# Optimization experiments

Measured on AMD Instinct MI355X. Metric: run time of the kernel, lower is better.

The kernel has to match this reference:

```python
import jax, jax.numpy as jnp
import numpy as np

N_NOTE = 14  # undefined global in original; must equal output_size for one-hot feedback


def setup_inputs() -> dict:
    key = jax.random.key(0)
    ks = jax.random.split(key, 9)
    B, T, H, O = 256, 512, 2048, 14
    s_i = 1.0 / np.sqrt(14)
    s_h = 1.0 / np.sqrt(H)
    return {
        "encoder_outputs": jax.random.normal(ks[0], (B, 1, H), jnp.float32),
        "encoder_hidden": jax.random.normal(ks[1], (1, B, H), jnp.float32),
        "target_tensor": jax.random.uniform(ks[2], (B, T, O), jnp.float32),
        "W_ih": jax.random.normal(ks[3], (3 * H, 14), jnp.float32) * s_i,
        "W_hh": jax.random.normal(ks[4], (3 * H, H), jnp.float32) * s_h,
        "b_ih": jax.random.normal(ks[5], (3 * H,), jnp.float32) * s_h,
        "b_hh": jax.random.normal(ks[6], (3 * H,), jnp.float32) * s_h,
        "W_out": jax.random.normal(ks[7], (O, H), jnp.float32) * s_h,
        "b_out": jax.random.normal(ks[8], (O,), jnp.float32) * s_h,
    }


def _decode(encoder_hidden, target_tensor, W_ih, W_hh, b_ih, b_hh, W_out, b_out):
    B, T, O = target_tensor.shape
    H = W_hh.shape[1]

    def step(carry, _):
        h, x = carry  # h: [B,H], x: [B,14]
        xr = jax.nn.relu(x)
        gi = xr @ W_ih.T + b_ih            # [B,3H]
        gh = h @ W_hh.T + b_hh             # [B,3H]
        r = jax.nn.sigmoid(gi[:, :H] + gh[:, :H])
        z = jax.nn.sigmoid(gi[:, H:2 * H] + gh[:, H:2 * H])
        n = jnp.tanh(gi[:, 2 * H:] + r * gh[:, 2 * H:])
        h_new = (1.0 - z) * n + z * h
        logits = h_new @ W_out.T + b_out   # [B,O]
        # feedback: one-hot of argmax; the Python `break` in the original zeros
        # every batch element at-or-after the first hit of n_note-1
        topi = jnp.argmax(logits, axis=-1)                     # [B]
        hit = (topi == N_NOTE - 1).astype(jnp.int32)
        alive = (jnp.cumsum(hit) == 0).astype(logits.dtype)    # inclusive cumsum
        x_next = jax.nn.one_hot(topi, O, dtype=logits.dtype) * alive[:, None]
        return (h_new, x_next), logits

    h0 = encoder_hidden[0]          # [B,H]
    x0 = target_tensor[:, 0]        # [B,14] first-step input
    (h_final, _), logits = jax.lax.scan(step, (h0, x0), None, length=T)
    logits = jnp.transpose(logits, (1, 0, 2))  # [B,T,O]
    log_probs = jax.nn.log_softmax(logits, axis=-1)
    return log_probs, h_final[None]  # ([B,T,O], [1,B,H])


def reference(encoder_outputs, encoder_hidden, target_tensor, W_ih, W_hh, b_ih, b_hh, W_out, b_out):
    # encoder_outputs is accepted but unused, matching the original forward
    return _decode(encoder_hidden, target_tensor, W_ih, W_hh, b_ih, b_hh, W_out, b_out)
```

## Files before the change

kernel.cpp:

```cpp
#include <hip/hip_runtime.h>
#include <math.h>

typedef float f4 __attribute__((ext_vector_type(4)));
typedef _Float16 f16x8 __attribute__((ext_vector_type(8)));
typedef _Float16 f16x4 __attribute__((ext_vector_type(4)));
typedef int i4 __attribute__((ext_vector_type(4)));

#define Hdim 2048
#define Bdim 256
#define Tdim 512
#define Odim 14
#define G3   6144


__global__ void prep_gtable(const float* __restrict__ b_ih,
                            const float* __restrict__ W_ih,
                            float* __restrict__ Gt) {
    int idx = blockIdx.x * 256 + threadIdx.x;
    if (idx >= 15 * G3) return;
    int c = idx / G3, row = idx % G3;
    float v = b_ih[row];
    if (c < Odim) v += W_ih[row * Odim + c];
    Gt[idx] = v;
}

__global__ void prep_gi0(const float* __restrict__ b_ih,
                         const float* __restrict__ W_ih,
                         const float* __restrict__ target,
                         float* __restrict__ gi0) {
    int idx = blockIdx.x * 256 + threadIdx.x;
    int b = idx / G3, row = idx % G3;
    const float* x0 = target + (size_t)b * (Tdim * Odim);
    float s = b_ih[row];
    #pragma unroll
    for (int c = 0; c < Odim; ++c)
        s = fmaf(fmaxf(x0[c], 0.f), W_ih[row * Odim + c], s);
    gi0[idx] = s;
}

__global__ void prep_Bpack(const float* __restrict__ W,
                           _Float16* __restrict__ Bh, _Float16* __restrict__ Bl) {
    int idx = blockIdx.x * 256 + threadIdx.x;
    int n = idx >> 8, kc = idx & 255;
    const float* src = W + (size_t)n * Hdim + kc * 8;
    int kb = kc >> 2, q = kc & 3;
    int lane = (n & 15) + 16 * q;
    int nt = n >> 4;
    f16x8 vh, vl;
    #pragma unroll
    for (int j = 0; j < 8; ++j) {
        float w = src[j];
        _Float16 h = (_Float16)w;
        vh[j] = h;
        vl[j] = (_Float16)(w - (float)h);
    }
    size_t off = (((size_t)nt * 64 + kb) * 64 + lane) * 8;
    *(f16x8*)(Bh + off) = vh;
    *(f16x8*)(Bl + off) = vl;
}

__global__ void prep_A0(const float* __restrict__ h0,
                        _Float16* __restrict__ Ah, _Float16* __restrict__ Al) {
    int idx = blockIdx.x * 256 + threadIdx.x;
    int m = idx >> 8, kc = idx & 255;
    const float* src = h0 + (size_t)m * Hdim + kc * 8;
    int kb = kc >> 2, q = kc & 3;
    int lane = (m & 15) + 16 * q;
    int mt = m >> 4;
    f16x8 vh, vl;
    #pragma unroll
    for (int j = 0; j < 8; ++j) {
        float w = src[j];
        _Float16 h = (_Float16)w;
        vh[j] = h;
        vl[j] = (_Float16)(w - (float)h);
    }
    size_t off = (((size_t)mt * 64 + kb) * 64 + lane) * 8;
    *(f16x8*)(Ah + off) = vh;
    *(f16x8*)(Al + off) = vl;
}

__global__ __launch_bounds__(512, 2)
void gemm_step(const _Float16* __restrict__ Ah, const _Float16* __restrict__ Al,
               const _Float16* __restrict__ Bh, const _Float16* __restrict__ Bl,
               float* __restrict__ Cpart) {
    __shared__ __align__(16) _Float16 sB[2][24576];

    const int tid = threadIdx.x;
    const int wave = tid >> 6, lane = tid & 63;
    const int nt0 = blockIdx.x * 3;
    const int kb0 = blockIdx.y * 32;

    f4 acc[2][3];
    #pragma unroll
    for (int mf = 0; mf < 2; ++mf)
        #pragma unroll
        for (int nf = 0; nf < 3; ++nf) acc[mf][nf] = (f4)0.f;

    i4 rh[3], rl[3];

    #pragma unroll
    for (int i = 0; i < 3; ++i) {
        int e = i * 512 + tid, blk = e >> 6, l = e & 63;
        int ntl = blk >> 3, kbl = blk & 7;
        size_t off = (((size_t)(nt0 + ntl) * 64) + kb0 + kbl) * 512 + l * 8;
        rh[i] = *(const i4*)(Bh + off);
        rl[i] = *(const i4*)(Bl + off);
    }
    #pragma unroll
    for (int i = 0; i < 3; ++i) {
        ((i4*)sB[0])[i * 512 + tid] = rh[i];
        ((i4*)sB[0])[1536 + i * 512 + tid] = rl[i];
    }
    __syncthreads();

    for (int c = 0; c < 4; ++c) {
        const int buf = c & 1;
        if (c < 3) {
            #pragma unroll
            for (int i = 0; i < 3; ++i) {
                int e = i * 512 + tid, blk = e >> 6, l = e & 63;
                int ntl = blk >> 3, kbl = blk & 7;
                size_t off = (((size_t)(nt0 + ntl) * 64) + kb0 + (c + 1) * 8 + kbl) * 512 + l * 8;
                rh[i] = *(const i4*)(Bh + off);
                rl[i] = *(const i4*)(Bl + off);
            }
        }
        #pragma unroll
        for (int kbl = 0; kbl < 8; ++kbl) {
            const int kb = kb0 + c * 8 + kbl;
            f16x8 a_h[2], a_l[2], b_h[3], b_l[3];
            #pragma unroll
            for (int mf = 0; mf < 2; ++mf) {
                size_t off = (((size_t)(wave * 2 + mf) * 64 + kb) * 64 + lane) * 8;
                a_h[mf] = *(const f16x8*)(Ah + off);
                a_l[mf] = *(const f16x8*)(Al + off);
            }
            #pragma unroll
            for (int nf = 0; nf < 3; ++nf) {
                int base = ((nf * 8 + kbl) * 64 + lane) * 8;
                b_h[nf] = *(const f16x8*)(&sB[buf][base]);
                b_l[nf] = *(const f16x8*)(&sB[buf][12288 + base]);
            }
            #pragma unroll
            for (int mf = 0; mf < 2; ++mf)
                #pragma unroll
                for (int nf = 0; nf < 3; ++nf) {
                    acc[mf][nf] = __builtin_amdgcn_mfma_f32_16x16x32_f16(
                        a_h[mf], b_h[nf], acc[mf][nf], 0, 0, 0);
                    acc[mf][nf] = __builtin_amdgcn_mfma_f32_16x16x32_f16(
                        a_h[mf], b_l[nf], acc[mf][nf], 0, 0, 0);
                    acc[mf][nf] = __builtin_amdgcn_mfma_f32_16x16x32_f16(
                        a_l[mf], b_h[nf], acc[mf][nf], 0, 0, 0);
                }
        }
        if (c < 3) {
            __syncthreads();
            #pragma unroll
            for (int i = 0; i < 3; ++i) {
                ((i4*)sB[buf ^ 1])[i * 512 + tid] = rh[i];
                ((i4*)sB[buf ^ 1])[1536 + i * 512 + tid] = rl[i];
            }
            __syncthreads();
        }
    }

    const size_t base = (size_t)blockIdx.y * Bdim * G3;
    #pragma unroll
    for (int mf = 0; mf < 2; ++mf) {
        int mrow = wave * 32 + mf * 16 + (lane >> 4) * 4;
        #pragma unroll
        for (int nf = 0; nf < 3; ++nf) {
            int n = (nt0 + nf) * 16 + (lane & 15);
            #pragma unroll
            for (int q = 0; q < 4; ++q)
                Cpart[base + (size_t)(mrow + q) * G3 + n] = acc[mf][nf][q];
        }
    }
}

__global__ __launch_bounds__(512)
void fused_out(const float* __restrict__ hprev, float* __restrict__ hnew,
               const float* __restrict__ Cpart, const float* __restrict__ Gt,
               const float* __restrict__ gi0, const float* __restrict__ b_hh,
               const float* __restrict__ W_out, const float* __restrict__ b_out,
               _Float16* __restrict__ Ah, _Float16* __restrict__ Al,
               const int* __restrict__ topi_in, int* __restrict__ topi_out,
               float* __restrict__ lp, float* __restrict__ hfin, int t) {
    const int b = blockIdx.x;
    const int tid = threadIdx.x;
    __shared__ __align__(16) float sh[Hdim];
    __shared__ float sl[16];
    __shared__ int s_sel;
    __shared__ unsigned long long s_m[4];

    if (t > 0) {
        if (tid < 256) {
            int tp = topi_in[tid];
            unsigned long long m = __ballot(tp == (Odim - 1));
            if ((tid & 63) == 0) s_m[tid >> 6] = m;
        }
        __syncthreads();
        if (tid == 0) {
            int bw = b >> 6, bl = b & 63;
            unsigned long long le =
                s_m[bw] & ((bl == 63) ? ~0ULL : ((1ULL << (bl + 1)) - 1ULL));
            bool dead = (le != 0ULL);
            for (int w = 0; w < bw; ++w) dead = dead || (s_m[w] != 0ULL);
            s_sel = dead ? Odim : topi_in[b];
        }
        __syncthreads();
    }
    const float* gp = (t == 0) ? (gi0 + (size_t)b * G3)
                               : (Gt + (size_t)s_sel * G3);

    const int j0 = tid * 4;
    float hn[4];
    {
        float gsum[3][4];
        #pragma unroll
        for (int g = 0; g < 3; ++g) {
            f4 s = *(const f4*)(b_hh + g * Hdim + j0);
            #pragma unroll
            for (int ks = 0; ks < 2; ++ks)
                s += *(const f4*)(Cpart + ((size_t)ks * Bdim + b) * G3 + g * Hdim + j0);
            #pragma unroll
            for (int c = 0; c < 4; ++c) gsum[g][c] = s[c];
        }
        f4 hp = *(const f4*)(hprev + (size_t)b * Hdim + j0);
        f4 gr = *(const f4*)(gp + j0);
        f4 gz = *(const f4*)(gp + Hdim + j0);
        f4 gn = *(const f4*)(gp + 2 * Hdim + j0);
        #pragma unroll
        for (int c = 0; c < 4; ++c) {
            float rr = 1.f / (1.f + expf(-(gr[c] + gsum[0][c])));
            float zz = 1.f / (1.f + expf(-(gz[c] + gsum[1][c])));
            float nn = tanhf(fmaf(rr, gsum[2][c], gn[c]));
            hn[c] = (1.f - zz) * nn + zz * hp[c];
        }
    }
    f4 o0;
    #pragma unroll
    for (int c = 0; c < 4; ++c) o0[c] = hn[c];
    *(f4*)(hnew + (size_t)b * Hdim + j0) = o0;
    {
        f16x4 vh, vl;
        #pragma unroll
        for (int c = 0; c < 4; ++c) {
            _Float16 hh = (_Float16)hn[c];
            vh[c] = hh;
            vl[c] = (_Float16)(hn[c] - (float)hh);
        }
        int kb = j0 >> 5, q = (j0 >> 3) & 3, e0 = j0 & 7;
        int lane = (b & 15) + 16 * q, mt = b >> 4;
        size_t off = (((size_t)mt * 64 + kb) * 64 + lane) * 8 + e0;
        *(f16x4*)(Ah + off) = vh;
        *(f16x4*)(Al + off) = vl;
    }
    *(f4*)(sh + j0) = o0;
    __syncthreads();

    const int w = tid >> 6, l = tid & 63;
    for (int o = w; o < Odim; o += 8) {
        const float* wo = W_out + (size_t)o * Hdim;
        float s = 0.f;
        #pragma unroll
        for (int i = 0; i < 32; ++i)
            s = fmaf(sh[l + 64 * i], wo[l + 64 * i], s);
        #pragma unroll
        for (int off = 32; off >= 1; off >>= 1)
            s += __shfl_down(s, off);
        if (l == 0) sl[o] = s + b_out[o];
    }
    __syncthreads();
    if (tid == 0) {
        float m = sl[0]; int bi = 0;
        #pragma unroll
        for (int o = 1; o < Odim; ++o)
            if (sl[o] > m) { m = sl[o]; bi = o; }
        float ssum = 0.f;
        #pragma unroll
        for (int o = 0; o < Odim; ++o) ssum += expf(sl[o] - m);
        topi_out[b] = bi;
        sl[14] = m + logf(ssum);
    }
    __syncthreads();
    if (tid < Odim)
        lp[(size_t)b * (Tdim * Odim) + (size_t)t * Odim + tid] = sl[tid] - sl[14];
    if (hfin)
        *(f4*)(hfin + (size_t)b * Hdim + j0) = o0;
}

extern "C" void kernel_launch(void* const* d_in, const int* in_sizes, int n_in,
                              void* d_out, int out_size, void* d_ws, size_t ws_size,
                              hipStream_t stream) {
    const float* enc_hidden = (const float*)d_in[1];
    const float* target     = (const float*)d_in[2];
    const float* W_ih       = (const float*)d_in[3];
    const float* W_hh       = (const float*)d_in[4];
    const float* b_ih       = (const float*)d_in[5];
    const float* b_hh       = (const float*)d_in[6];
    const float* W_out      = (const float*)d_in[7];
    const float* b_out      = (const float*)d_in[8];

    float* out  = (float*)d_out;
    float* lp   = out;
    float* hfin = out + (size_t)Bdim * Tdim * Odim;

    float* ws    = (float*)d_ws;
    float* hb0   = ws;
    float* hb1   = hb0 + 524288;
    float* Gt    = hb1 + 524288;
    float* gi0   = Gt + 15 * G3;
    float* Cpart = gi0 + (size_t)Bdim * G3;
    _Float16* Ah = (_Float16*)(Cpart + 4 * (size_t)Bdim * G3);
    _Float16* Al = Ah + (size_t)Bdim * Hdim;
    _Float16* Bh = Al + (size_t)Bdim * Hdim;
    _Float16* Bl = Bh + (size_t)G3 * Hdim;
    int* topibuf = (int*)(Bl + (size_t)G3 * Hdim);

    prep_gtable<<<(15 * G3 + 255) / 256, 256, 0, stream>>>(b_ih, W_ih, Gt);
    prep_gi0<<<(Bdim * G3) / 256, 256, 0, stream>>>(b_ih, W_ih, target, gi0);
    prep_Bpack<<<(G3 * 256) / 256, 256, 0, stream>>>(W_hh, Bh, Bl);
    prep_A0<<<(Bdim * 256) / 256, 256, 0, stream>>>(enc_hidden, Ah, Al);

    for (int t = 0; t < Tdim; ++t) {
        float* hnew = (t & 1) ? hb1 : hb0;
        const float* hprev = (t == 0) ? enc_hidden : ((t & 1) ? hb0 : hb1);
        int* tin  = topibuf + ((t + 1) & 1) * 256;
        int* tout = topibuf + (t & 1) * 256;
        gemm_step<<<dim3(128, 2), 512, 0, stream>>>(Ah, Al, Bh, Bl, Cpart);
        fused_out<<<256, 512, 0, stream>>>(hprev, hnew, Cpart, Gt, gi0, b_hh,
                                           W_out, b_out, Ah, Al, tin, tout, lp,
                                           (t == Tdim - 1) ? hfin : nullptr, t);
    }
}
```

Before: 19.46 ms.

## Split GEMM K four ways and stage B tiles via direct global-to-LDS loads

The per-step recurrent GEMM's split-K factor goes from 2 to 4, so the grid doubles to 512 blocks, and each block handles 16 K-blocks in chunks of 4. Shared memory per block is halved and launch bounds allow 4 blocks per CU. B staging moves from register round-trips to global_load_lds async copies, which removes the extra syncthreads and register pressure. In exchange, fused_out must read and sum four partial buffers instead of two, which adds memory traffic on the reduce side.

```diff
diff --git a/kernel.cpp b/kernel.cpp
--- a/kernel.cpp
+++ b/kernel.cpp
@@ -80,16 +80,16 @@
     *(f16x8*)(Al + off) = vl;
 }
 
-__global__ __launch_bounds__(512, 2)
+__global__ __launch_bounds__(512, 4)
 void gemm_step(const _Float16* __restrict__ Ah, const _Float16* __restrict__ Al,
                const _Float16* __restrict__ Bh, const _Float16* __restrict__ Bl,
                float* __restrict__ Cpart) {
-    __shared__ __align__(16) _Float16 sB[2][24576];
+    __shared__ __align__(16) _Float16 sB[2][12288];
 
     const int tid = threadIdx.x;
     const int wave = tid >> 6, lane = tid & 63;
     const int nt0 = blockIdx.x * 3;
-    const int kb0 = blockIdx.y * 32;
+    const int kb0 = blockIdx.y * 16;
 
     f4 acc[2][3];
     #pragma unroll
@@ -97,38 +97,32 @@
         #pragma unroll
         for (int nf = 0; nf < 3; ++nf) acc[mf][nf] = (f4)0.f;
 
-    i4 rh[3], rl[3];
-
-    #pragma unroll
-    for (int i = 0; i < 3; ++i) {
-        int e = i * 512 + tid, blk = e >> 6, l = e & 63;
-        int ntl = blk >> 3, kbl = blk & 7;
-        size_t off = (((size_t)(nt0 + ntl) * 64) + kb0 + kbl) * 512 + l * 8;
-        rh[i] = *(const i4*)(Bh + off);
-        rl[i] = *(const i4*)(Bl + off);
-    }
-    #pragma unroll
-    for (int i = 0; i < 3; ++i) {
-        ((i4*)sB[0])[i * 512 + tid] = rh[i];
-        ((i4*)sB[0])[1536 + i * 512 + tid] = rl[i];
-    }
+    auto stage = [&](int buf, int c) {
+        #pragma unroll
+        for (int i = 0; i < 3; ++i) {
+            int e = i * 512 + tid;
+            int half = (e >= 768) ? 1 : 0;
+            int r = e - half * 768;
+            int blk = r >> 6, l = e & 63;
+            int ntl = blk >> 2, kbl = blk & 3;
+            const _Float16* src = (half ? Bl : Bh) +
+                ((((size_t)(nt0 + ntl) * 64) + kb0 + c * 4 + kbl) * 512 + l * 8);
+            __builtin_amdgcn_global_load_lds(
+                (const __attribute__((address_space(1))) void*)src,
+                (__attribute__((address_space(3))) void*)(&sB[buf][(size_t)e * 8]),
+                16, 0, 0);
+        }
+    };
+
+    stage(0, 0);
     __syncthreads();
 
     for (int c = 0; c < 4; ++c) {
         const int buf = c & 1;
-        if (c < 3) {
-            #pragma unroll
-            for (int i = 0; i < 3; ++i) {
-                int e = i * 512 + tid, blk = e >> 6, l = e & 63;
-                int ntl = blk >> 3, kbl = blk & 7;
-                size_t off = (((size_t)(nt0 + ntl) * 64) + kb0 + (c + 1) * 8 + kbl) * 512 + l * 8;
-                rh[i] = *(const i4*)(Bh + off);
-                rl[i] = *(const i4*)(Bl + off);
-            }
-        }
-        #pragma unroll
-        for (int kbl = 0; kbl < 8; ++kbl) {
-            const int kb = kb0 + c * 8 + kbl;
+        if (c < 3) stage(buf ^ 1, c + 1);
+        #pragma unroll
+        for (int kbl = 0; kbl < 4; ++kbl) {
+            const int kb = kb0 + c * 4 + kbl;
             f16x8 a_h[2], a_l[2], b_h[3], b_l[3];
             #pragma unroll
             for (int mf = 0; mf < 2; ++mf) {
@@ -138,9 +132,9 @@
             }
             #pragma unroll
             for (int nf = 0; nf < 3; ++nf) {
-                int base = ((nf * 8 + kbl) * 64 + lane) * 8;
+                int base = ((nf * 4 + kbl) * 64 + lane) * 8;
                 b_h[nf] = *(const f16x8*)(&sB[buf][base]);
-                b_l[nf] = *(const f16x8*)(&sB[buf][12288 + base]);
+                b_l[nf] = *(const f16x8*)(&sB[buf][6144 + base]);
             }
             #pragma unroll
             for (int mf = 0; mf < 2; ++mf)
@@ -154,15 +148,7 @@
                         a_l[mf], b_h[nf], acc[mf][nf], 0, 0, 0);
                 }
         }
-        if (c < 3) {
-            __syncthreads();
-            #pragma unroll
-            for (int i = 0; i < 3; ++i) {
-                ((i4*)sB[buf ^ 1])[i * 512 + tid] = rh[i];
-                ((i4*)sB[buf ^ 1])[1536 + i * 512 + tid] = rl[i];
-            }
-            __syncthreads();
-        }
+        __syncthreads();
     }
 
     const size_t base = (size_t)blockIdx.y * Bdim * G3;
@@ -222,7 +208,7 @@
         for (int g = 0; g < 3; ++g) {
             f4 s = *(const f4*)(b_hh + g * Hdim + j0);
             #pragma unroll
-            for (int ks = 0; ks < 2; ++ks)
+            for (int ks = 0; ks < 4; ++ks)
                 s += *(const f4*)(Cpart + ((size_t)ks * Bdim + b) * G3 + g * Hdim + j0);
             #pragma unroll
             for (int c = 0; c < 4; ++c) gsum[g][c] = s[c];
@@ -329,7 +315,7 @@
         const float* hprev = (t == 0) ? enc_hidden : ((t & 1) ? hb0 : hb1);
         int* tin  = topibuf + ((t + 1) & 1) * 256;
         int* tout = topibuf + (t & 1) * 256;
-        gemm_step<<<dim3(128, 2), 512, 0, stream>>>(Ah, Al, Bh, Bl, Cpart);
+        gemm_step<<<dim3(128, 4), 512, 0, stream>>>(Ah, Al, Bh, Bl, Cpart);
         fused_out<<<256, 512, 0, stream>>>(hprev, hnew, Cpart, Gt, gi0, b_hh,
                                            W_out, b_out, Ah, Al, tin, tout, lp,
                                            (t == Tdim - 1) ? hfin : nullptr, t);
```

New measurement: 18.87 ms. -3.0%, faster.
